# Performance work log

Measured on AMD Instinct MI355X. Metric: run time of the kernel, lower is better.

Reference implementation:

```python
import jax, jax.numpy as jnp
import numpy as np

TOP_K = 4
NEG_N = 5
NEG_SEED = 1234  # fixed seed replacing python random.sample for determinism


def setup_inputs() -> dict:
    key = jax.random.key(0)
    k1, k2, k3 = jax.random.split(key, 3)
    B, D, R, S = 16, 256, 1024, 20
    vit_feature = jax.random.normal(k1, (B, D, R), dtype=jnp.float32)
    lag_feature = jax.random.normal(k2, (B, S, D), dtype=jnp.float32)
    lag_vit_map = jax.random.normal(k3, (B, S, R), dtype=jnp.float32)
    return {"vit_feature": vit_feature, "lag_feature": lag_feature,
            "lag_vit_map": lag_vit_map}


def reference(vit_feature, lag_feature, lag_vit_map):
    # permutes from the original torch code
    m = jnp.transpose(lag_vit_map, (0, 2, 1))    # (B, R, S)
    vit = jnp.transpose(vit_feature, (0, 2, 1))  # (B, R, D)
    lag_tok = lag_feature                        # (B, S, D): token kk's feature is lag[b][:, kk] after permute == lag_feature[b, kk, :]
    B, R, D = vit.shape

    # topk language tokens per visual row
    _, cols = jax.lax.top_k(m, TOP_K)            # (B, R, TOP_K) int32 indices into S

    # vit_corrspondence_feature[jj] = stack_b vit[b, jj, :]  -> (R, B, D)
    vit_corr = jnp.transpose(vit, (1, 0, 2))

    # lag_corrspondence_feature[jj][b] = stack_k lag_tok[b, cols[b,jj,k], :] -> (R, B, K, D)
    gather_tok = jax.vmap(lambda t, c: t[c])     # t:(S,D), c:(R,K) -> (R,K,D)
    lag_corr = jnp.transpose(gather_tok(lag_tok, cols), (1, 0, 2, 3))

    # negatives: original code's inner loop only keeps the LAST batch index (B-1).
    # It samples NEG_N rows without replacement from range(R), excluding jj when
    # that index equals ii (here ii == B-1 for the surviving sample is only
    # relevant when the outer ii == B-1; exclusion is applied on the diagonal).
    skey = jax.random.key(NEG_SEED)
    scores = jax.random.uniform(skey, (R, B, R))          # random scores for sampling w/o replacement
    rr = jnp.arange(R)
    scores = scores.at[rr, B - 1, rr].set(-1.0)           # exclude jj for ii == B-1
    _, neg_idx = jax.lax.top_k(scores, NEG_N)             # (R, B, NEG_N)
    neg = vit[B - 1][neg_idx]                             # (R, B, NEG_N, D)

    return vit_corr, lag_corr, neg
```

## Files before the change

### kernel.cpp

```cpp
#include <hip/hip_runtime.h>
#include <stdint.h>

#define R_DIM 1024
#define B_DIM 16
#define D_DIM 256
#define S_DIM 20

__device__ __forceinline__ void threefry2x32_1234(uint32_t x0, uint32_t x1,
                                                  uint32_t& o0, uint32_t& o1) {
  const uint32_t ks1 = 1234u;
  const uint32_t ks2 = 1234u ^ 0x1BD11BDAu;
  x1 += ks1;
#define TF_ROUND(r) { x0 += x1; x1 = (x1 << (r)) | (x1 >> (32 - (r))); x1 ^= x0; }
  TF_ROUND(13) TF_ROUND(15) TF_ROUND(26) TF_ROUND(6)
  x0 += ks1; x1 += ks2 + 1u;
  TF_ROUND(17) TF_ROUND(29) TF_ROUND(16) TF_ROUND(24)
  x0 += ks2; x1 += 2u;
  TF_ROUND(13) TF_ROUND(15) TF_ROUND(26) TF_ROUND(6)
  x1 += ks1 + 3u;
  TF_ROUND(17) TF_ROUND(29) TF_ROUND(16) TF_ROUND(24)
  x0 += ks1; x1 += ks2 + 4u;
  TF_ROUND(13) TF_ROUND(15) TF_ROUND(26) TF_ROUND(6)
  x0 += ks2; x1 += 5u;
#undef TF_ROUND
  o0 = x0; o1 = x1;
}

__device__ __forceinline__ unsigned long long wave_max_u64(unsigned long long v) {
#pragma unroll
  for (int off = 1; off < 64; off <<= 1) {
    unsigned long long o = __shfl_xor(v, off, 64);
    v = (o > v) ? o : v;
  }
  return v;
}

__global__ __launch_bounds__(256) void k1_transpose(const float* __restrict__ vit,
                                                    float* __restrict__ out0) {
  __shared__ float tile[32][33];
  const int b = blockIdx.z;
  const int r0 = blockIdx.x * 32;
  const int d0 = blockIdx.y * 32;
  const int tx = threadIdx.x, ty = threadIdx.y;
  const float* src = vit + (size_t)b * D_DIM * R_DIM;
#pragma unroll
  for (int i = 0; i < 4; ++i) {
    int d = d0 + ty + i * 8;
    tile[ty + i * 8][tx] = src[(size_t)d * R_DIM + r0 + tx];
  }
  __syncthreads();
#pragma unroll
  for (int i = 0; i < 4; ++i) {
    int r = r0 + ty + i * 8;
    out0[((size_t)r * B_DIM + b) * D_DIM + d0 + tx] = tile[tx][ty + i * 8];
  }
}

__global__ __launch_bounds__(256) void k2_lag(const float* __restrict__ lag_feature,
                                              const float* __restrict__ lag_vit_map,
                                              float* __restrict__ out1) {
  const int tid = blockIdx.x * blockDim.x + threadIdx.x;
  const int lane = threadIdx.x & 63;
  const int row = tid >> 6;
  const int r = row >> 4;
  const int b = row & 15;

  unsigned long long key = 0ull;
  if (lane < S_DIM) {
    float f = lag_vit_map[((size_t)b * S_DIM + lane) * R_DIM + r];
    uint32_t u = __float_as_uint(f);
    uint32_t ok = u ^ (uint32_t)(((int32_t)u >> 31) | 0x80000000u);
    key = ((unsigned long long)ok << 32) | (0xFFFFFFFFu - (uint32_t)lane);
  }

  uint32_t cols[4];
#pragma unroll
  for (int k = 0; k < 4; ++k) {
    unsigned long long m = wave_max_u64(key);
    cols[k] = 0xFFFFFFFFu - (uint32_t)m;
    if (key == m) key = 0ull;
  }

#pragma unroll
  for (int k = 0; k < 4; ++k) {
    const float4* src = (const float4*)(lag_feature + ((size_t)b * S_DIM + cols[k]) * D_DIM);
    float4* dst = (float4*)(out1 + ((size_t)row * 4 + k) * D_DIM);
    dst[lane] = src[lane];
  }
}

__device__ __forceinline__ void top5_mask(unsigned long long* keys, uint32_t* idx) {
#pragma unroll
  for (int n = 0; n < 5; ++n) {
    unsigned long long lm = keys[0];
#pragma unroll
    for (int t = 1; t < 16; ++t) lm = (keys[t] > lm) ? keys[t] : lm;
    unsigned long long g = wave_max_u64(lm);
    idx[n] = 0xFFFFFFFFu - (uint32_t)g;
#pragma unroll
    for (int t = 0; t < 16; ++t)
      if (keys[t] == g) keys[t] = 0ull;
  }
}

__global__ __launch_bounds__(256) void k3_neg(const float* __restrict__ out0,
                                              float* __restrict__ out2) {
  const int tid = blockIdx.x * blockDim.x + threadIdx.x;
  const int lane = threadIdx.x & 63;
  const int row = tid >> 6;
  const int r = row >> 4, b = row & 15;

  unsigned long long keys[16];
  const uint32_t base = (uint32_t)row * 1024u;
#pragma unroll
  for (int t = 0; t < 16; ++t) {
    uint32_t s = (uint32_t)lane + ((uint32_t)t << 6);
    uint32_t o0, o1;
    threefry2x32_1234(0u, base + s, o0, o1);
    uint32_t bits = o0 ^ o1;
    unsigned long long k =
        ((unsigned long long)(bits >> 9) << 32) | (0xFFFFFFFFu - s);
    if (b == 15 && s == (uint32_t)r) k = 0ull;
    keys[t] = k;
  }

  uint32_t idx[5];
  top5_mask(keys, idx);

#pragma unroll
  for (int n = 0; n < 5; ++n) {
    const float4* src = (const float4*)(out0 + ((size_t)idx[n] * B_DIM + 15) * D_DIM);
    float4* dst = (float4*)(out2 + ((size_t)row * 5 + n) * D_DIM);
    dst[lane] = src[lane];
  }
}

extern "C" void kernel_launch(void* const* d_in, const int* in_sizes, int n_in,
                              void* d_out, int out_size, void* d_ws, size_t ws_size,
                              hipStream_t stream) {
  (void)in_sizes; (void)n_in; (void)d_ws; (void)ws_size; (void)out_size;
  const float* vit = (const float*)d_in[0];
  const float* lag = (const float*)d_in[1];
  const float* map = (const float*)d_in[2];
  float* out = (float*)d_out;
  float* out0 = out;
  float* out1 = out + 4194304;
  float* out2 = out + 4194304 + 16777216;

  dim3 g1(R_DIM / 32, D_DIM / 32, B_DIM), b1(32, 8);
  k1_transpose<<<g1, b1, 0, stream>>>(vit, out0);
  k2_lag<<<4096, 256, 0, stream>>>(lag, map, out1);
  k3_neg<<<4096, 256, 0, stream>>>(out0, out2);
}
```

Baseline: 218.4 us.

## Merge transpose and lag gather into one launch; use nontemporal stores

```diff
diff --git a/kernel.cpp b/kernel.cpp
--- a/kernel.cpp
+++ b/kernel.cpp
@@ -5,6 +5,8 @@
 #define B_DIM 16
 #define D_DIM 256
 #define S_DIM 20
+
+typedef float f32x4 __attribute__((ext_vector_type(4)));
 
 __device__ __forceinline__ void threefry2x32_1234(uint32_t x0, uint32_t x1,
                                                   uint32_t& o0, uint32_t& o1) {
@@ -35,57 +37,69 @@
   return v;
 }
 
-__global__ __launch_bounds__(256) void k1_transpose(const float* __restrict__ vit,
-                                                    float* __restrict__ out0) {
-  __shared__ float tile[32][33];
-  const int b = blockIdx.z;
-  const int r0 = blockIdx.x * 32;
-  const int d0 = blockIdx.y * 32;
-  const int tx = threadIdx.x, ty = threadIdx.y;
-  const float* src = vit + (size_t)b * D_DIM * R_DIM;
+__global__ __launch_bounds__(256) void kA(const float* __restrict__ vit,
+                                          const float* __restrict__ lag_feature,
+                                          const float* __restrict__ lag_vit_map,
+                                          float* __restrict__ out0,
+                                          float* __restrict__ out1) {
+  if (blockIdx.x < 4096) {
+    __shared__ float tile[32][33];
+    const int id = blockIdx.x;
+    const int bx = id & 31;
+    const int by = (id >> 5) & 7;
+    const int bz = id >> 8;
+    const int r0 = bx * 32, d0 = by * 32;
+    const int tx = threadIdx.x & 31, ty = threadIdx.x >> 5;
+    const float* src = vit + (size_t)bz * D_DIM * R_DIM;
 #pragma unroll
-  for (int i = 0; i < 4; ++i) {
-    int d = d0 + ty + i * 8;
-    tile[ty + i * 8][tx] = src[(size_t)d * R_DIM + r0 + tx];
-  }
-  __syncthreads();
+    for (int i = 0; i < 4; ++i) {
+      int d = d0 + ty + i * 8;
+      tile[ty + i * 8][tx] = src[(size_t)d * R_DIM + r0 + tx];
+    }
+    __syncthreads();
+    if (bz == 15) {
 #pragma unroll
-  for (int i = 0; i < 4; ++i) {
-    int r = r0 + ty + i * 8;
-    out0[((size_t)r * B_DIM + b) * D_DIM + d0 + tx] = tile[tx][ty + i * 8];
-  }
-}
+      for (int i = 0; i < 4; ++i) {
+        int r = r0 + ty + i * 8;
+        out0[((size_t)r * B_DIM + bz) * D_DIM + d0 + tx] = tile[tx][ty + i * 8];
+      }
+    } else {
+#pragma unroll
+      for (int i = 0; i < 4; ++i) {
+        int r = r0 + ty + i * 8;
+        __builtin_nontemporal_store(tile[tx][ty + i * 8],
+                                    &out0[((size_t)r * B_DIM + bz) * D_DIM + d0 + tx]);
+      }
+    }
+  } else {
+    const int tid = (blockIdx.x - 4096) * 256 + threadIdx.x;
+    const int lane = threadIdx.x & 63;
+    const int row = tid >> 6;
+    const int r = row >> 4;
+    const int b = row & 15;
 
-__global__ __launch_bounds__(256) void k2_lag(const float* __restrict__ lag_feature,
-                                              const float* __restrict__ lag_vit_map,
-                                              float* __restrict__ out1) {
-  const int tid = blockIdx.x * blockDim.x + threadIdx.x;
-  const int lane = threadIdx.x & 63;
-  const int row = tid >> 6;
-  const int r = row >> 4;
-  const int b = row & 15;
+    unsigned long long key = 0ull;
+    if (lane < S_DIM) {
+      float f = lag_vit_map[((size_t)b * S_DIM + lane) * R_DIM + r];
+      uint32_t u = __float_as_uint(f);
+      uint32_t ok = u ^ (uint32_t)(((int32_t)u >> 31) | 0x80000000u);
+      key = ((unsigned long long)ok << 32) | (0xFFFFFFFFu - (uint32_t)lane);
+    }
 
-  unsigned long long key = 0ull;
-  if (lane < S_DIM) {
-    float f = lag_vit_map[((size_t)b * S_DIM + lane) * R_DIM + r];
-    uint32_t u = __float_as_uint(f);
-    uint32_t ok = u ^ (uint32_t)(((int32_t)u >> 31) | 0x80000000u);
-    key = ((unsigned long long)ok << 32) | (0xFFFFFFFFu - (uint32_t)lane);
-  }
-
-  uint32_t cols[4];
+    uint32_t cols[4];
 #pragma unroll
-  for (int k = 0; k < 4; ++k) {
-    unsigned long long m = wave_max_u64(key);
-    cols[k] = 0xFFFFFFFFu - (uint32_t)m;
-    if (key == m) key = 0ull;
-  }
+    for (int k = 0; k < 4; ++k) {
+      unsigned long long m = wave_max_u64(key);
+      cols[k] = 0xFFFFFFFFu - (uint32_t)m;
+      if (key == m) key = 0ull;
+    }
 
 #pragma unroll
-  for (int k = 0; k < 4; ++k) {
-    const float4* src = (const float4*)(lag_feature + ((size_t)b * S_DIM + cols[k]) * D_DIM);
-    float4* dst = (float4*)(out1 + ((size_t)row * 4 + k) * D_DIM);
-    dst[lane] = src[lane];
+    for (int k = 0; k < 4; ++k) {
+      const f32x4* src = (const f32x4*)(lag_feature + ((size_t)b * S_DIM + cols[k]) * D_DIM);
+      f32x4* dst = (f32x4*)(out1 + ((size_t)row * 4 + k) * D_DIM);
+      __builtin_nontemporal_store(src[lane], &dst[lane]);
+    }
   }
 }
 
@@ -103,8 +117,8 @@
   }
 }
 
-__global__ __launch_bounds__(256) void k3_neg(const float* __restrict__ out0,
-                                              float* __restrict__ out2) {
+__global__ __launch_bounds__(256) void kB(const float* __restrict__ out0,
+                                          float* __restrict__ out2) {
   const int tid = blockIdx.x * blockDim.x + threadIdx.x;
   const int lane = threadIdx.x & 63;
   const int row = tid >> 6;
@@ -129,9 +143,9 @@
 
 #pragma unroll
   for (int n = 0; n < 5; ++n) {
-    const float4* src = (const float4*)(out0 + ((size_t)idx[n] * B_DIM + 15) * D_DIM);
-    float4* dst = (float4*)(out2 + ((size_t)row * 5 + n) * D_DIM);
-    dst[lane] = src[lane];
+    const f32x4* src = (const f32x4*)(out0 + ((size_t)idx[n] * B_DIM + 15) * D_DIM);
+    f32x4* dst = (f32x4*)(out2 + ((size_t)row * 5 + n) * D_DIM);
+    __builtin_nontemporal_store(src[lane], &dst[lane]);
   }
 }
 
@@ -147,8 +161,6 @@
   float* out1 = out + 4194304;
   float* out2 = out + 4194304 + 16777216;
 
-  dim3 g1(R_DIM / 32, D_DIM / 32, B_DIM), b1(32, 8);
-  k1_transpose<<<g1, b1, 0, stream>>>(vit, out0);
-  k2_lag<<<4096, 256, 0, stream>>>(lag, map, out1);
-  k3_neg<<<4096, 256, 0, stream>>>(out0, out2);
+  kA<<<8192, 256, 0, stream>>>(vit, lag, map, out0, out1);
+  kB<<<4096, 256, 0, stream>>>(out0, out2);
 }
```

Measured after the change: 218.3 us. No clear change (-0.1%).
